# Optimization experiments

Measured on AMD Instinct MI355X. Metric: run time of the kernel, lower is better.

Reference implementation:

```python
import jax, jax.numpy as jnp
import numpy as np

NEG_SLOPE = 0.2   # PyG GATConv default negative_slope
BN_EPS = 1e-5


def gat_layer(x, src, dst, W, a_src, a_dst, b, num_nodes):
    """PyG-style GATConv (concat=True). src/dst already include self-loops."""
    H, C = a_src.shape
    h = (x @ W).reshape(num_nodes, H, C)            # [N,H,C]
    al_s = jnp.sum(h * a_src, axis=-1)              # [N,H] per-node src score
    al_d = jnp.sum(h * a_dst, axis=-1)              # [N,H]
    e = al_s[src] + al_d[dst]                       # [E,H]
    e = jnp.where(e > 0, e, NEG_SLOPE * e)          # leaky_relu
    m = jax.ops.segment_max(e, dst, num_segments=num_nodes)
    e = jnp.exp(e - m[dst])
    s = jax.ops.segment_sum(e, dst, num_segments=num_nodes)
    alpha = e / (s[dst] + 1e-16)                    # segment softmax over dst
    out = jax.ops.segment_sum(alpha[:, :, None] * h[src], dst, num_segments=num_nodes)
    return out.reshape(num_nodes, H * C) + b


def batch_norm(x, gamma, beta):
    mu = jnp.mean(x, axis=0)
    var = jnp.mean((x - mu) ** 2, axis=0)
    return (x - mu) * jax.lax.rsqrt(var + BN_EPS) * gamma + beta


def setup_inputs() -> dict:
    N, E, IN, H, C, L, OUT, NC = 50000, 800000, 256, 4, 64, 32, 32, 30
    HC = H * C
    key = jax.random.key(0)
    cnt = [0]
    def nk():
        cnt[0] += 1
        return jax.random.fold_in(key, cnt[0])
    def w(shape, scale):
        return jax.random.normal(nk(), shape, jnp.float32) * scale
    inp = {
        "x": jax.random.normal(nk(), (N, IN), jnp.float32),
        "edge_index": jax.random.randint(nk(), (2, E), 0, N, dtype=jnp.int32),
        "eps": jax.random.normal(nk(), (N, L), jnp.float32),
    }
    for i, d_in in zip((1, 2, 3), (IN, HC, HC)):
        inp[f"W{i}"] = w((d_in, HC), 1.0 / np.sqrt(d_in))
        inp[f"asrc{i}"] = w((H, C), 0.1)
        inp[f"adst{i}"] = w((H, C), 0.1)
        inp[f"b{i}"] = jnp.zeros((HC,), jnp.float32)
        inp[f"g{i}"] = jnp.ones((HC,), jnp.float32)
        inp[f"be{i}"] = jnp.zeros((HC,), jnp.float32)
    inp["Wr"] = w((IN, HC), 1.0 / np.sqrt(IN)); inp["br"] = jnp.zeros((HC,), jnp.float32)
    inp["Wmu"] = w((HC, L), 1.0 / np.sqrt(HC)); inp["bmu"] = jnp.zeros((L,), jnp.float32)
    inp["Wlv"] = w((HC, L), 1.0 / np.sqrt(HC)); inp["blv"] = jnp.zeros((L,), jnp.float32)
    inp["Wd"] = w((L, OUT), 1.0 / np.sqrt(L)); inp["bd"] = jnp.zeros((OUT,), jnp.float32)
    inp["Wa"] = w((HC, NC), 1.0 / np.sqrt(HC)); inp["ba"] = jnp.zeros((NC,), jnp.float32)
    return inp


def reference(x, edge_index, eps,
              W1, asrc1, adst1, b1, g1, be1,
              W2, asrc2, adst2, b2, g2, be2,
              W3, asrc3, adst3, b3, g3, be3,
              Wr, br, Wmu, bmu, Wlv, blv, Wd, bd, Wa, ba):
    N = x.shape[0]
    loop = jnp.arange(N, dtype=edge_index.dtype)   # PyG add_self_loops default
    src = jnp.concatenate([edge_index[0], loop])
    dst = jnp.concatenate([edge_index[1], loop])

    residual = x @ Wr + br                          # [N, HC]
    h = jax.nn.relu(batch_norm(gat_layer(x, src, dst, W1, asrc1, adst1, b1, N), g1, be1))
    h = jax.nn.relu(batch_norm(gat_layer(h, src, dst, W2, asrc2, adst2, b2, N), g2, be2))
    h = jax.nn.relu(batch_norm(gat_layer(h, src, dst, W3, asrc3, adst3, b3, N), g3, be3))
    enc = h + residual

    mu = enc @ Wmu + bmu
    logvar = enc @ Wlv + blv
    z = mu + eps * jnp.exp(0.5 * logvar)            # reparameterize
    out = z @ Wd + bd
    aux_out = enc @ Wa + ba
    return (out, mu, logvar, aux_out, enc)
```

## Files before the change

kernel.cpp:

```cpp
#include <hip/hip_runtime.h>
#include <cstdint>

typedef __bf16 bf16;
typedef __bf16 bf16x8 __attribute__((ext_vector_type(8)));
typedef float f32x4 __attribute__((ext_vector_type(4)));
typedef _Float16 fp16;
typedef _Float16 half8 __attribute__((ext_vector_type(8)));

#define NEG_SLOPE 0.2f
#define BN_EPS 1e-5f

__device__ __forceinline__ void gld_lds16(const void* g, void* l) {
  auto gp = reinterpret_cast<const __attribute__((address_space(1))) unsigned int*>(
      reinterpret_cast<uintptr_t>(g));
  auto lp = reinterpret_cast<__attribute__((address_space(3))) unsigned int*>(
      reinterpret_cast<uintptr_t>(l));
  __builtin_amdgcn_global_load_lds(gp, lp, 16, 0, 0);
}

__global__ void k_init_counts(int* counts, int N) {
  int i = blockIdx.x * 256 + threadIdx.x;
  if (i < N) counts[i] = 1;
}

__global__ void k_count(const int* __restrict__ ei, int* counts, int E) {
  int i = blockIdx.x * 256 + threadIdx.x;
  if (i < E) atomicAdd(&counts[ei[E + i]], 1);
}

__global__ __launch_bounds__(256) void k_scan1(const int* __restrict__ counts,
                                               int* __restrict__ row_start,
                                               int* __restrict__ bsums, int N) {
  __shared__ int s[256];
  const int t = threadIdx.x;
  const int idx = blockIdx.x * 1024 + t * 4;
  int a0 = (idx + 0 < N) ? counts[idx + 0] : 0;
  int a1 = (idx + 1 < N) ? counts[idx + 1] : 0;
  int a2 = (idx + 2 < N) ? counts[idx + 2] : 0;
  int a3 = (idx + 3 < N) ? counts[idx + 3] : 0;
  const int mysum = a0 + a1 + a2 + a3;
  s[t] = mysum;
  __syncthreads();
  for (int ofs = 1; ofs < 256; ofs <<= 1) {
    int v = (t >= ofs) ? s[t - ofs] : 0;
    __syncthreads();
    s[t] += v;
    __syncthreads();
  }
  int excl = s[t] - mysum;
  if (idx + 0 < N) row_start[idx + 0] = excl;
  if (idx + 1 < N) row_start[idx + 1] = excl + a0;
  if (idx + 2 < N) row_start[idx + 2] = excl + a0 + a1;
  if (idx + 3 < N) row_start[idx + 3] = excl + a0 + a1 + a2;
  if (t == 255) bsums[blockIdx.x] = s[255];
}

__global__ void k_scan2(int* __restrict__ bsums, int* __restrict__ row_start, int nb, int N) {
  if (threadIdx.x == 0 && blockIdx.x == 0) {
    int run = 0;
    for (int i = 0; i < nb; ++i) {
      int v = bsums[i];
      bsums[i] = run;
      run += v;
    }
    row_start[N] = run;
  }
}

__global__ void k_scan3(int* __restrict__ row_start, int* __restrict__ cursor,
                        const int* __restrict__ bsums, int N) {
  int i = blockIdx.x * 256 + threadIdx.x;
  if (i < N) {
    int v = row_start[i] + bsums[i >> 10];
    row_start[i] = v;
    cursor[i] = v;
  }
}

__global__ void k_fill(const int* __restrict__ ei, int* cursor, int* __restrict__ csr_src,
                       int E, int N) {
  int i = blockIdx.x * 256 + threadIdx.x;
  if (i < E) {
    int s = ei[i], d = ei[E + i];
    int p = atomicAdd(&cursor[d], 1);
    csr_src[p] = s;
  } else if (i < E + N) {
    int n = i - E;
    int p = atomicAdd(&cursor[n], 1);
    csr_src[p] = n;
  }
}

__global__ void k_split(const float* __restrict__ src, bf16* __restrict__ hi,
                        bf16* __restrict__ lo, int n) {
  int i = blockIdx.x * 256 + threadIdx.x;
  if (i < n) {
    float v = src[i];
    bf16 h = (bf16)v;
    hi[i] = h;
    lo[i] = (bf16)(v - (float)h);
  }
}

__global__ void k_transpose_w(const float* __restrict__ W, bf16* __restrict__ Wth,
                              bf16* __restrict__ Wtl) {
  int k = blockIdx.x, n = threadIdx.x;
  float v = W[k * 256 + n];
  bf16 h = (bf16)v;
  Wth[n * 256 + k] = h;
  Wtl[n * 256 + k] = (bf16)(v - (float)h);
}

__global__ void k_build_head_w(const float* __restrict__ Wmu, const float* __restrict__ bmu,
                               const float* __restrict__ Wlv, const float* __restrict__ blv,
                               const float* __restrict__ Wa, const float* __restrict__ ba,
                               bf16* __restrict__ Whh, bf16* __restrict__ Whl,
                               float* __restrict__ bias_cat) {
  int k = blockIdx.x, n = threadIdx.x;
  float v = 0.f;
  if (n < 32) v = Wmu[k * 32 + n];
  else if (n < 64) v = Wlv[k * 32 + (n - 32)];
  else if (n < 94) v = Wa[k * 30 + (n - 64)];
  bf16 h = (bf16)v;
  Whh[n * 256 + k] = h;
  Whl[n * 256 + k] = (bf16)(v - (float)h);
  if (k == 0) {
    float b = 0.f;
    if (n < 32) b = bmu[n];
    else if (n < 64) b = blv[n - 32];
    else if (n < 94) b = ba[n - 64];
    bias_cat[n] = b;
  }
}

__global__ __launch_bounds__(256) void k_gemm(
    const bf16* __restrict__ Ah, const bf16* __restrict__ Al,
    const bf16* __restrict__ Bh, const bf16* __restrict__ Bl,
    const float* __restrict__ bias, float* __restrict__ Cf, fp16* __restrict__ C16,
    const float* __restrict__ asrcp, const float* __restrict__ adstp,
    float* __restrict__ alsp, float* __restrict__ aldp,
    int M, int ldc) {
  __shared__ bf16 Ash[128 * 32];
  __shared__ bf16 Asl[128 * 32];
  __shared__ bf16 Bsh[128 * 32];
  __shared__ bf16 Bsl[128 * 32];
  const int t = threadIdx.x;
  const int wave = t >> 6, lane = t & 63;
  const int m0 = blockIdx.x * 128, n0 = blockIdx.y * 128;
  const int lrow = lane & 15, lq = lane >> 4;
  const int wm = (wave >> 1) * 64, wn = (wave & 1) * 64;

  f32x4 acc[4][4] = {};

  const int j0 = wave * 64 + lane, j1 = j0 + 256;
  const int ar0 = j0 >> 2, ar1 = j1 >> 2;
  const int ak0 = ((j0 & 3) ^ ((ar0 >> 1) & 3)) * 8;
  const int ak1 = ((j1 & 3) ^ ((ar1 >> 1) & 3)) * 8;
  const int gm0 = min(m0 + ar0, M - 1), gm1 = min(m0 + ar1, M - 1);
  const size_t oa0 = (size_t)gm0 * 256 + ak0, oa1 = (size_t)gm1 * 256 + ak1;
  const size_t ob0 = (size_t)(n0 + ar0) * 256 + ak0, ob1 = (size_t)(n0 + ar1) * 256 + ak1;
  const int l0 = wave * 512, l1 = 2048 + wave * 512;

  for (int k0 = 0; k0 < 256; k0 += 32) {
    __syncthreads();
    gld_lds16(Ah + oa0 + k0, Ash + l0);
    gld_lds16(Ah + oa1 + k0, Ash + l1);
    gld_lds16(Al + oa0 + k0, Asl + l0);
    gld_lds16(Al + oa1 + k0, Asl + l1);
    gld_lds16(Bh + ob0 + k0, Bsh + l0);
    gld_lds16(Bh + ob1 + k0, Bsh + l1);
    gld_lds16(Bl + ob0 + k0, Bsl + l0);
    gld_lds16(Bl + ob1 + k0, Bsl + l1);
    __syncthreads();
    bf16x8 afh[4], afl[4], bfh[4], bfl[4];
#pragma unroll
    for (int mi = 0; mi < 4; mi++) {
      int row = wm + mi * 16 + lrow;
      int off = row * 32 + ((lq ^ ((row >> 1) & 3)) << 3);
      afh[mi] = *(const bf16x8*)(Ash + off);
      afl[mi] = *(const bf16x8*)(Asl + off);
    }
#pragma unroll
    for (int ni = 0; ni < 4; ni++) {
      int row = wn + ni * 16 + lrow;
      int off = row * 32 + ((lq ^ ((row >> 1) & 3)) << 3);
      bfh[ni] = *(const bf16x8*)(Bsh + off);
      bfl[ni] = *(const bf16x8*)(Bsl + off);
    }
#pragma unroll
    for (int mi = 0; mi < 4; mi++)
#pragma unroll
      for (int ni = 0; ni < 4; ni++) {
        acc[mi][ni] = __builtin_amdgcn_mfma_f32_16x16x32_bf16(afl[mi], bfh[ni], acc[mi][ni], 0, 0, 0);
        acc[mi][ni] = __builtin_amdgcn_mfma_f32_16x16x32_bf16(afh[mi], bfl[ni], acc[mi][ni], 0, 0, 0);
        acc[mi][ni] = __builtin_amdgcn_mfma_f32_16x16x32_bf16(afh[mi], bfh[ni], acc[mi][ni], 0, 0, 0);
      }
  }

#pragma unroll
  for (int mi = 0; mi < 4; mi++) {
    const int mb = m0 + wm + mi * 16 + lq * 4;
#pragma unroll
    for (int ni = 0; ni < 4; ni++) {
      const int n = n0 + wn + ni * 16 + lrow;
#pragma unroll
      for (int r = 0; r < 4; r++) {
        int m = mb + r;
        if (m < M) {
          if (C16) C16[(size_t)m * ldc + n] = (fp16)acc[mi][ni][r];
          else     Cf[(size_t)m * ldc + n] = acc[mi][ni][r] + (bias ? bias[n] : 0.f);
        }
      }
    }
  }

  if (asrcp) {
    const int headg = (n0 + wn) >> 6;
    float as4[4], ad4[4];
#pragma unroll
    for (int ni = 0; ni < 4; ni++) {
      int cg = n0 + wn + ni * 16 + lrow;
      as4[ni] = asrcp[cg];
      ad4[ni] = adstp[cg];
    }
#pragma unroll
    for (int mi = 0; mi < 4; mi++) {
      float ps[4] = {0.f, 0.f, 0.f, 0.f}, pd[4] = {0.f, 0.f, 0.f, 0.f};
#pragma unroll
      for (int ni = 0; ni < 4; ni++)
#pragma unroll
        for (int r = 0; r < 4; r++) {
          ps[r] += acc[mi][ni][r] * as4[ni];
          pd[r] += acc[mi][ni][r] * ad4[ni];
        }
#pragma unroll
      for (int o = 1; o < 16; o <<= 1)
#pragma unroll
        for (int r = 0; r < 4; r++) {
          ps[r] += __shfl_xor(ps[r], o, 64);
          pd[r] += __shfl_xor(pd[r], o, 64);
        }
      if (lrow == 0) {
#pragma unroll
        for (int r = 0; r < 4; r++) {
          int m = m0 + wm + mi * 16 + lq * 4 + r;
          if (m < M) {
            alsp[(size_t)m * 4 + headg] = ps[r];
            aldp[(size_t)m * 4 + headg] = pd[r];
          }
        }
      }
    }
  }
}

__global__ __launch_bounds__(256) void k_gather(
    const fp16* __restrict__ h16, const float* __restrict__ als, const float* __restrict__ ald,
    const int* __restrict__ row_start, const int* __restrict__ csr_src,
    const float* __restrict__ bias, fp16* __restrict__ out, float* __restrict__ stats, int N) {
  if (blockIdx.x == 0) { stats[threadIdx.x] = 0.f; stats[256 + threadIdx.x] = 0.f; }
  const int wave = threadIdx.x >> 6, lane = threadIdx.x & 63;
  const int half = lane >> 5, l32 = lane & 31;
  const int n = blockIdx.x * 8 + wave * 2 + half;
  if (n >= N) return;
  const int head = l32 >> 3;
  const int c0 = l32 * 8;
  const float adh = ald[(size_t)n * 4 + head];
  const int beg = row_start[n], end = row_start[n + 1];
  float s = 0.f;
  float acc[8] = {0.f, 0.f, 0.f, 0.f, 0.f, 0.f, 0.f, 0.f};
#pragma unroll 4
  for (int i = beg; i < end; ++i) {
    const int sidx = csr_src[i];
    float e = als[(size_t)sidx * 4 + head] + adh;
    e = e > 0.f ? e : NEG_SLOPE * e;
    const float w = __expf(e);
    s += w;
    const half8 hv = *(const half8*)(h16 + (size_t)sidx * 256 + c0);
#pragma unroll
    for (int k = 0; k < 8; ++k) acc[k] += w * (float)hv[k];
  }
  const float inv = 1.f / (s + 1e-16f);
  const float4 b1 = *(const float4*)(bias + c0);
  const float4 b2 = *(const float4*)(bias + c0 + 4);
  half8 o;
  o[0] = (fp16)(acc[0] * inv + b1.x); o[1] = (fp16)(acc[1] * inv + b1.y);
  o[2] = (fp16)(acc[2] * inv + b1.z); o[3] = (fp16)(acc[3] * inv + b1.w);
  o[4] = (fp16)(acc[4] * inv + b2.x); o[5] = (fp16)(acc[5] * inv + b2.y);
  o[6] = (fp16)(acc[6] * inv + b2.z); o[7] = (fp16)(acc[7] * inv + b2.w);
  *(half8*)(out + (size_t)n * 256 + c0) = o;
}

__global__ __launch_bounds__(256) void k_bn_stats(const fp16* __restrict__ x,
                                                  float* __restrict__ stats, int N) {
  const int t = threadIdx.x;
  int r0 = blockIdx.x * 128;
  int rend = min(r0 + 128, N);
  float s = 0.f, sq = 0.f;
  for (int r = r0; r < rend; ++r) {
    float v = (float)x[(size_t)r * 256 + t];
    s += v; sq += v * v;
  }
  atomicAdd(&stats[t], s);
  atomicAdd(&stats[256 + t], sq);
}

__global__ __launch_bounds__(256) void k_bn_apply(
    const fp16* __restrict__ x, const float* __restrict__ stats,
    const float* __restrict__ g, const float* __restrict__ be,
    bf16* __restrict__ act_hi, bf16* __restrict__ act_lo, float* __restrict__ encf,
    float invN, int total) {
  int idx = blockIdx.x * 256 + threadIdx.x;
  if (idx >= total) return;
  int c = idx & 255;
  float mu = stats[c] * invN;
  float var = stats[256 + c] * invN - mu * mu;
  float v = ((float)x[idx] - mu) * rsqrtf(var + BN_EPS) * g[c] + be[c];
  v = fmaxf(v, 0.f);
  if (encf) { v += encf[idx]; encf[idx] = v; }
  bf16 h = (bf16)v;
  act_hi[idx] = h;
  act_lo[idx] = (bf16)(v - (float)h);
}

__global__ __launch_bounds__(256) void k_finish(
    const float* __restrict__ HEAD, const float* __restrict__ eps,
    const float* __restrict__ Wd, const float* __restrict__ bd,
    float* __restrict__ o_out, float* __restrict__ o_mu, float* __restrict__ o_lv,
    float* __restrict__ o_aux, int N) {
  __shared__ float sWd[1024];
  __shared__ float sZ[8][33];
  const int t = threadIdx.x;
  for (int i = t; i < 1024; i += 256) sWd[i] = Wd[i];
  __syncthreads();
  const int r = t >> 5, j = t & 31;
  const int n = blockIdx.x * 8 + r;
  if (n < N) {
    const float* hp = HEAD + (size_t)n * 128;
    float mu = hp[j];
    float lv = hp[32 + j];
    float z = mu + eps[(size_t)n * 32 + j] * __expf(0.5f * lv);
    sZ[r][j] = z;
    o_mu[(size_t)n * 32 + j] = mu;
    o_lv[(size_t)n * 32 + j] = lv;
    if (j < 30) o_aux[(size_t)n * 30 + j] = hp[64 + j];
  }
  __syncthreads();
  if (n < N) {
    float o = bd[j];
#pragma unroll
    for (int k = 0; k < 32; ++k) o += sZ[r][k] * sWd[k * 32 + j];
    o_out[(size_t)n * 32 + j] = o;
  }
}

extern "C" void kernel_launch(void* const* d_in, const int* in_sizes, int n_in,
                              void* d_out, int out_size, void* d_ws, size_t ws_size,
                              hipStream_t stream) {
  const float* x   = (const float*)d_in[0];
  const int*   ei  = (const int*)d_in[1];
  const float* eps = (const float*)d_in[2];
  const float* Wg[3]   = {(const float*)d_in[3], (const float*)d_in[9],  (const float*)d_in[15]};
  const float* asrc[3] = {(const float*)d_in[4], (const float*)d_in[10], (const float*)d_in[16]};
  const float* adst[3] = {(const float*)d_in[5], (const float*)d_in[11], (const float*)d_in[17]};
  const float* bg[3]   = {(const float*)d_in[6], (const float*)d_in[12], (const float*)d_in[18]};
  const float* gam[3]  = {(const float*)d_in[7], (const float*)d_in[13], (const float*)d_in[19]};
  const float* bet[3]  = {(const float*)d_in[8], (const float*)d_in[14], (const float*)d_in[20]};
  const float* Wr  = (const float*)d_in[21];
  const float* br  = (const float*)d_in[22];
  const float* Wmu = (const float*)d_in[23];
  const float* bmu = (const float*)d_in[24];
  const float* Wlv = (const float*)d_in[25];
  const float* blv = (const float*)d_in[26];
  const float* Wd  = (const float*)d_in[27];
  const float* bd  = (const float*)d_in[28];
  const float* Wa  = (const float*)d_in[29];
  const float* ba  = (const float*)d_in[30];

  const int N = in_sizes[0] / 256;
  const int E = in_sizes[1] / 2;

  float* outp  = (float*)d_out;
  float* o_out = outp;
  float* o_mu  = outp + (size_t)N * 32;
  float* o_lv  = outp + (size_t)N * 64;
  float* o_aux = outp + (size_t)N * 96;
  float* o_enc = outp + (size_t)N * 96 + (size_t)N * 30;

  char* p = (char*)d_ws;
  auto carve = [&](size_t bytes) -> char* {
    char* r = p;
    p += (bytes + 255) & ~(size_t)255;
    return r;
  };
  int* counts    = (int*)carve((size_t)N * 4);
  int* row_start = (int*)carve(((size_t)N + 1) * 4);
  int* cursor    = (int*)carve((size_t)N * 4);
  int* csr_src   = (int*)carve((size_t)(E + N) * 4);
  int* bsums     = (int*)carve(((size_t)N / 1024 + 2) * 4);
  bf16* Wth[4];
  bf16* Wtl[4];
  for (int i = 0; i < 4; ++i) {
    Wth[i] = (bf16*)carve(256 * 256 * 2);
    Wtl[i] = (bf16*)carve(256 * 256 * 2);
  }
  bf16* Whh = (bf16*)carve(128 * 256 * 2);
  bf16* Whl = (bf16*)carve(128 * 256 * 2);
  float* bias_cat = (float*)carve(128 * 4);
  bf16* Ahi = (bf16*)carve((size_t)N * 256 * 2);
  bf16* Alo = (bf16*)carve((size_t)N * 256 * 2);
  fp16* H16 = (fp16*)carve((size_t)N * 256 * 2);
  float* FHEAD = (float*)carve((size_t)N * 128 * 4);
  fp16* AGG16 = (fp16*)carve((size_t)N * 256 * 2);
  float* als = (float*)carve((size_t)N * 4 * 4);
  float* ald = (float*)carve((size_t)N * 4 * 4);
  float* stats = (float*)carve(512 * 4);

  dim3 b256(256);

  const int nb_scan = (N + 1023) / 1024;
  k_init_counts<<<(N + 255) / 256, b256, 0, stream>>>(counts, N);
  k_count<<<(E + 255) / 256, b256, 0, stream>>>(ei, counts, E);
  k_scan1<<<nb_scan, b256, 0, stream>>>(counts, row_start, bsums, N);
  k_scan2<<<1, 64, 0, stream>>>(bsums, row_start, nb_scan, N);
  k_scan3<<<(N + 255) / 256, b256, 0, stream>>>(row_start, cursor, bsums, N);
  k_fill<<<(E + N + 255) / 256, b256, 0, stream>>>(ei, cursor, csr_src, E, N);

  k_split<<<((size_t)N * 256 + 255) / 256, b256, 0, stream>>>(x, Ahi, Alo, N * 256);
  k_transpose_w<<<256, b256, 0, stream>>>(Wr, Wth[0], Wtl[0]);
  for (int l = 0; l < 3; ++l)
    k_transpose_w<<<256, b256, 0, stream>>>(Wg[l], Wth[l + 1], Wtl[l + 1]);
  k_build_head_w<<<256, dim3(128), 0, stream>>>(Wmu, bmu, Wlv, blv, Wa, ba, Whh, Whl, bias_cat);

  dim3 ggrid((N + 127) / 128, 2);
  k_gemm<<<ggrid, b256, 0, stream>>>(Ahi, Alo, Wth[0], Wtl[0], br, o_enc, nullptr,
                                     nullptr, nullptr, nullptr, nullptr, N, 256);

  const float invN = 1.0f / (float)N;
  for (int l = 0; l < 3; ++l) {
    k_gemm<<<ggrid, b256, 0, stream>>>(Ahi, Alo, Wth[l + 1], Wtl[l + 1], nullptr, nullptr, H16,
                                       asrc[l], adst[l], als, ald, N, 256);
    k_gather<<<(N + 7) / 8, b256, 0, stream>>>(H16, als, ald, row_start, csr_src, bg[l],
                                               AGG16, stats, N);
    k_bn_stats<<<(N + 127) / 128, b256, 0, stream>>>(AGG16, stats, N);
    if (l < 2)
      k_bn_apply<<<((size_t)N * 256 + 255) / 256, b256, 0, stream>>>(
          AGG16, stats, gam[l], bet[l], Ahi, Alo, nullptr, invN, N * 256);
    else
      k_bn_apply<<<((size_t)N * 256 + 255) / 256, b256, 0, stream>>>(
          AGG16, stats, gam[l], bet[l], Ahi, Alo, o_enc, invN, N * 256);
  }

  dim3 hgrid((N + 127) / 128, 1);
  k_gemm<<<hgrid, b256, 0, stream>>>(Ahi, Alo, Whh, Whl, bias_cat, FHEAD, nullptr,
                                     nullptr, nullptr, nullptr, nullptr, N, 128);
  k_finish<<<(N + 7) / 8, b256, 0, stream>>>(FHEAD, eps, Wd, bd, o_out, o_mu, o_lv, o_aux, N);
}
```

Baseline: 886.9 us.

## Split feature buffer by head pairs and fuse BN stats into gather

```diff
diff --git a/kernel.cpp b/kernel.cpp
--- a/kernel.cpp
+++ b/kernel.cpp
@@ -6,6 +6,7 @@
 typedef float f32x4 __attribute__((ext_vector_type(4)));
 typedef _Float16 fp16;
 typedef _Float16 half8 __attribute__((ext_vector_type(8)));
+typedef _Float16 half4 __attribute__((ext_vector_type(4)));
 
 #define NEG_SLOPE 0.2f
 #define BN_EPS 1e-5f
@@ -136,15 +137,20 @@
 __global__ __launch_bounds__(256) void k_gemm(
     const bf16* __restrict__ Ah, const bf16* __restrict__ Al,
     const bf16* __restrict__ Bh, const bf16* __restrict__ Bl,
-    const float* __restrict__ bias, float* __restrict__ Cf, fp16* __restrict__ C16,
+    const float* __restrict__ bias, float* __restrict__ Cf,
+    fp16* __restrict__ C16a, fp16* __restrict__ C16b,
     const float* __restrict__ asrcp, const float* __restrict__ adstp,
-    float* __restrict__ alsp, float* __restrict__ aldp,
+    float* __restrict__ alsp, float* __restrict__ aldp, float* __restrict__ statsz,
     int M, int ldc) {
   __shared__ bf16 Ash[128 * 32];
   __shared__ bf16 Asl[128 * 32];
   __shared__ bf16 Bsh[128 * 32];
   __shared__ bf16 Bsl[128 * 32];
   const int t = threadIdx.x;
+  if (statsz && blockIdx.x == 0 && blockIdx.y == 0) {
+    statsz[t] = 0.f;
+    statsz[256 + t] = 0.f;
+  }
   const int wave = t >> 6, lane = t & 63;
   const int m0 = blockIdx.x * 128, n0 = blockIdx.y * 128;
   const int lrow = lane & 15, lq = lane >> 4;
@@ -207,8 +213,12 @@
       for (int r = 0; r < 4; r++) {
         int m = mb + r;
         if (m < M) {
-          if (C16) C16[(size_t)m * ldc + n] = (fp16)acc[mi][ni][r];
-          else     Cf[(size_t)m * ldc + n] = acc[mi][ni][r] + (bias ? bias[n] : 0.f);
+          if (C16a) {
+            fp16* dst = (n & 128) ? C16b : C16a;
+            dst[(size_t)m * 128 + (n & 127)] = (fp16)acc[mi][ni][r];
+          } else {
+            Cf[(size_t)m * ldc + n] = acc[mi][ni][r] + (bias ? bias[n] : 0.f);
+          }
         }
       }
     }
@@ -255,54 +265,56 @@
 }
 
 __global__ __launch_bounds__(256) void k_gather(
-    const fp16* __restrict__ h16, const float* __restrict__ als, const float* __restrict__ ald,
+    const fp16* __restrict__ hA, const fp16* __restrict__ hB,
+    const float* __restrict__ als, const float* __restrict__ ald,
     const int* __restrict__ row_start, const int* __restrict__ csr_src,
     const float* __restrict__ bias, fp16* __restrict__ out, float* __restrict__ stats, int N) {
-  if (blockIdx.x == 0) { stats[threadIdx.x] = 0.f; stats[256 + threadIdx.x] = 0.f; }
-  const int wave = threadIdx.x >> 6, lane = threadIdx.x & 63;
+  __shared__ float sm[128], sq[128];
+  const int t = threadIdx.x;
+  if (t < 128) { sm[t] = 0.f; sq[t] = 0.f; }
+  __syncthreads();
+  const int hc = blockIdx.y;
+  const fp16* __restrict__ hbuf = hc ? hB : hA;
+  const int wave = t >> 6, lane = t & 63;
   const int half = lane >> 5, l32 = lane & 31;
   const int n = blockIdx.x * 8 + wave * 2 + half;
-  if (n >= N) return;
-  const int head = l32 >> 3;
-  const int c0 = l32 * 8;
-  const float adh = ald[(size_t)n * 4 + head];
-  const int beg = row_start[n], end = row_start[n + 1];
-  float s = 0.f;
-  float acc[8] = {0.f, 0.f, 0.f, 0.f, 0.f, 0.f, 0.f, 0.f};
+  const int cl = l32 * 4;
+  if (n < N) {
+    const int head = hc * 2 + (l32 >> 4);
+    const float adh = ald[(size_t)n * 4 + head];
+    const int beg = row_start[n], end = row_start[n + 1];
+    float s = 0.f;
+    float a0 = 0.f, a1 = 0.f, a2 = 0.f, a3 = 0.f;
 #pragma unroll 4
-  for (int i = beg; i < end; ++i) {
-    const int sidx = csr_src[i];
-    float e = als[(size_t)sidx * 4 + head] + adh;
-    e = e > 0.f ? e : NEG_SLOPE * e;
-    const float w = __expf(e);
-    s += w;
-    const half8 hv = *(const half8*)(h16 + (size_t)sidx * 256 + c0);
-#pragma unroll
-    for (int k = 0; k < 8; ++k) acc[k] += w * (float)hv[k];
-  }
-  const float inv = 1.f / (s + 1e-16f);
-  const float4 b1 = *(const float4*)(bias + c0);
-  const float4 b2 = *(const float4*)(bias + c0 + 4);
-  half8 o;
-  o[0] = (fp16)(acc[0] * inv + b1.x); o[1] = (fp16)(acc[1] * inv + b1.y);
-  o[2] = (fp16)(acc[2] * inv + b1.z); o[3] = (fp16)(acc[3] * inv + b1.w);
-  o[4] = (fp16)(acc[4] * inv + b2.x); o[5] = (fp16)(acc[5] * inv + b2.y);
-  o[6] = (fp16)(acc[6] * inv + b2.z); o[7] = (fp16)(acc[7] * inv + b2.w);
-  *(half8*)(out + (size_t)n * 256 + c0) = o;
-}
-
-__global__ __launch_bounds__(256) void k_bn_stats(const fp16* __restrict__ x,
-                                                  float* __restrict__ stats, int N) {
-  const int t = threadIdx.x;
-  int r0 = blockIdx.x * 128;
-  int rend = min(r0 + 128, N);
-  float s = 0.f, sq = 0.f;
-  for (int r = r0; r < rend; ++r) {
-    float v = (float)x[(size_t)r * 256 + t];
-    s += v; sq += v * v;
-  }
-  atomicAdd(&stats[t], s);
-  atomicAdd(&stats[256 + t], sq);
+    for (int i = beg; i < end; ++i) {
+      const int sidx = csr_src[i];
+      float e = als[(size_t)sidx * 4 + head] + adh;
+      e = e > 0.f ? e : NEG_SLOPE * e;
+      const float w = __expf(e);
+      s += w;
+      const half4 hv = *(const half4*)(hbuf + (size_t)sidx * 128 + cl);
+      a0 += w * (float)hv[0];
+      a1 += w * (float)hv[1];
+      a2 += w * (float)hv[2];
+      a3 += w * (float)hv[3];
+    }
+    const float inv = 1.f / (s + 1e-16f);
+    const float4 b = *(const float4*)(bias + hc * 128 + cl);
+    const float v0 = a0 * inv + b.x, v1 = a1 * inv + b.y;
+    const float v2 = a2 * inv + b.z, v3 = a3 * inv + b.w;
+    half4 o;
+    o[0] = (fp16)v0; o[1] = (fp16)v1; o[2] = (fp16)v2; o[3] = (fp16)v3;
+    *(half4*)(out + (size_t)n * 256 + hc * 128 + cl) = o;
+    atomicAdd(&sm[cl + 0], v0); atomicAdd(&sq[cl + 0], v0 * v0);
+    atomicAdd(&sm[cl + 1], v1); atomicAdd(&sq[cl + 1], v1 * v1);
+    atomicAdd(&sm[cl + 2], v2); atomicAdd(&sq[cl + 2], v2 * v2);
+    atomicAdd(&sm[cl + 3], v3); atomicAdd(&sq[cl + 3], v3 * v3);
+  }
+  __syncthreads();
+  if (t < 128) {
+    atomicAdd(&stats[hc * 128 + t], sm[t]);
+    atomicAdd(&stats[256 + hc * 128 + t], sq[t]);
+  }
 }
 
 __global__ __launch_bounds__(256) void k_bn_apply(
@@ -409,7 +421,8 @@
   float* bias_cat = (float*)carve(128 * 4);
   bf16* Ahi = (bf16*)carve((size_t)N * 256 * 2);
   bf16* Alo = (bf16*)carve((size_t)N * 256 * 2);
-  fp16* H16 = (fp16*)carve((size_t)N * 256 * 2);
+  fp16* H16A = (fp16*)carve((size_t)N * 128 * 2);
+  fp16* H16B = (fp16*)carve((size_t)N * 128 * 2);
   float* FHEAD = (float*)carve((size_t)N * 128 * 4);
   fp16* AGG16 = (fp16*)carve((size_t)N * 256 * 2);
   float* als = (float*)carve((size_t)N * 4 * 4);
@@ -433,16 +446,16 @@
   k_build_head_w<<<256, dim3(128), 0, stream>>>(Wmu, bmu, Wlv, blv, Wa, ba, Whh, Whl, bias_cat);
 
   dim3 ggrid((N + 127) / 128, 2);
-  k_gemm<<<ggrid, b256, 0, stream>>>(Ahi, Alo, Wth[0], Wtl[0], br, o_enc, nullptr,
-                                     nullptr, nullptr, nullptr, nullptr, N, 256);
+  dim3 ggather((N + 7) / 8, 2);
+  k_gemm<<<ggrid, b256, 0, stream>>>(Ahi, Alo, Wth[0], Wtl[0], br, o_enc, nullptr, nullptr,
+                                     nullptr, nullptr, nullptr, nullptr, nullptr, N, 256);
 
   const float invN = 1.0f / (float)N;
   for (int l = 0; l < 3; ++l) {
-    k_gemm<<<ggrid, b256, 0, stream>>>(Ahi, Alo, Wth[l + 1], Wtl[l + 1], nullptr, nullptr, H16,
-                                       asrc[l], adst[l], als, ald, N, 256);
-    k_gather<<<(N + 7) / 8, b256, 0, stream>>>(H16, als, ald, row_start, csr_src, bg[l],
-                                               AGG16, stats, N);
-    k_bn_stats<<<(N + 127) / 128, b256, 0, stream>>>(AGG16, stats, N);
+    k_gemm<<<ggrid, b256, 0, stream>>>(Ahi, Alo, Wth[l + 1], Wtl[l + 1], nullptr, nullptr,
+                                       H16A, H16B, asrc[l], adst[l], als, ald, stats, N, 256);
+    k_gather<<<ggather, b256, 0, stream>>>(H16A, H16B, als, ald, row_start, csr_src, bg[l],
+                                           AGG16, stats, N);
     if (l < 2)
       k_bn_apply<<<((size_t)N * 256 + 255) / 256, b256, 0, stream>>>(
           AGG16, stats, gam[l], bet[l], Ahi, Alo, nullptr, invN, N * 256);
@@ -452,7 +465,7 @@
   }
 
   dim3 hgrid((N + 127) / 128, 1);
-  k_gemm<<<hgrid, b256, 0, stream>>>(Ahi, Alo, Whh, Whl, bias_cat, FHEAD, nullptr,
-                                     nullptr, nullptr, nullptr, nullptr, N, 128);
+  k_gemm<<<hgrid, b256, 0, stream>>>(Ahi, Alo, Whh, Whl, bias_cat, FHEAD, nullptr, nullptr,
+                                     nullptr, nullptr, nullptr, nullptr, nullptr, N, 128);
   k_finish<<<(N + 7) / 8, b256, 0, stream>>>(FHEAD, eps, Wd, bd, o_out, o_mu, o_lv, o_aux, N);
 }
```

Measured after the change: 1.575 ms. 77.5% more time.
